# Kernel tuning notes

Measured on AMD Instinct MI355X. Metric: run time of the kernel, lower is better.

Reference implementation:

```python
import jax, jax.numpy as jnp
import numpy as np

B, N, C = 16, 1024, 384
HEADS = 4
HIDDEN = 4 * C  # mlp_ratio=4 -> 1536
EPS = 1e-5


def layernorm(x, g, b):
    mu = jnp.mean(x, axis=-1, keepdims=True)
    var = jnp.mean((x - mu) ** 2, axis=-1, keepdims=True)
    return (x - mu) / jnp.sqrt(var + EPS) * g + b


def hardswish(x):
    return x * jnp.clip(x + 3.0, 0.0, 6.0) / 6.0


def setup_inputs() -> dict:
    key = jax.random.key(0)
    ks = jax.random.split(key, 8)
    s = 0.02
    return {
        "x": jax.random.normal(ks[0], (B, N, C), jnp.float32),
        "ln1_g": jnp.ones((C,), jnp.float32),
        "ln1_b": jnp.zeros((C,), jnp.float32),
        "Wqkv": jax.random.normal(ks[1], (3 * C, C), jnp.float32) * s,
        "Wproj": jax.random.normal(ks[2], (C, C), jnp.float32) * s,
        "bproj": jnp.zeros((C,), jnp.float32),
        "ln2_g": jnp.ones((C,), jnp.float32),
        "ln2_b": jnp.zeros((C,), jnp.float32),
        "Wfc1": jax.random.normal(ks[3], (HIDDEN, C, 1, 1), jnp.float32) * s,
        "bfc1": jnp.zeros((HIDDEN,), jnp.float32),
        "Wdw": jax.random.normal(ks[4], (HIDDEN, 1, 3, 3), jnp.float32) * s,
        "bdw": jnp.zeros((HIDDEN,), jnp.float32),
        "Wfc2": jax.random.normal(ks[5], (C, HIDDEN, 1, 1), jnp.float32) * s,
        "bfc2": jnp.zeros((C,), jnp.float32),
        "H": 32,
        "W": 32,
    }


def reference(x, ln1_g, ln1_b, Wqkv, Wproj, bproj, ln2_g, ln2_b,
              Wfc1, bfc1, Wdw, bdw, Wfc2, bfc2, H, W):
    b, n, c = x.shape
    h = HEADS
    hd = c // h
    # --- attention branch ---
    xn = layernorm(x, ln1_g, ln1_b)
    qkv = xn @ Wqkv.T  # [B,N,3C]
    qkv = qkv.reshape(b, n, h, 3, hd).transpose(3, 0, 2, 1, 4)  # [3,B,h,N,hd]
    q, k, v = qkv[0], qkv[1], qkv[2]
    attn = jax.nn.softmax(jnp.einsum('bhnd,bhmd->bhnm', q, k) * (hd ** -0.5), axis=-1)
    o = jnp.einsum('bhnm,bhmd->bhnd', attn, v)  # [B,h,N,hd]
    o = o.transpose(0, 2, 1, 3).reshape(b, n, c)
    o = o @ Wproj.T + bproj
    x = x + o
    # --- IRB (inverted residual conv MLP) branch ---
    y = layernorm(x, ln2_g, ln2_b)
    y = y.transpose(0, 2, 1).reshape(b, c, H, W)  # NCHW
    dn = ('NCHW', 'OIHW', 'NCHW')
    y = jax.lax.conv_general_dilated(y, Wfc1, (1, 1), 'VALID', dimension_numbers=dn)
    y = hardswish(y + bfc1[None, :, None, None])
    y = jax.lax.conv_general_dilated(y, Wdw, (1, 1), 'SAME',
                                     feature_group_count=Wdw.shape[0],
                                     dimension_numbers=dn)
    y = hardswish(y + bdw[None, :, None, None])
    y = jax.lax.conv_general_dilated(y, Wfc2, (1, 1), 'VALID', dimension_numbers=dn)
    y = y + bfc2[None, :, None, None]
    y = y.reshape(b, c, n).transpose(0, 2, 1)
    return x + y
```

## Files before the change

### kernel.cpp

```cpp
#include <hip/hip_runtime.h>
#include <hip/hip_bf16.h>
#include <math.h>

#define BB 16
#define NN 1024
#define CC 384
#define HEADS 4
#define HD 96
#define HID 1536
#define MROWS (BB*NN)

typedef __attribute__((ext_vector_type(8))) short bf16x8;
typedef __attribute__((ext_vector_type(4))) float f32x4;

__device__ __forceinline__ float hswish(float x) {
    float t = fminf(fmaxf(x + 3.0f, 0.0f), 6.0f);
    return x * t * (1.0f / 6.0f);
}

__device__ __forceinline__ ushort f2bf(float f) {
    union { float f; unsigned u; } v; v.f = f;
    unsigned r = v.u + 0x7fff + ((v.u >> 16) & 1);
    return (ushort)(r >> 16);
}

__device__ __forceinline__ float bf2f(ushort u) {
    union { unsigned u; float f; } v; v.u = ((unsigned)u) << 16;
    return v.f;
}

__device__ __forceinline__ void gload16(const ushort* g, ushort* l) {
    __builtin_amdgcn_global_load_lds(
        (const __attribute__((address_space(1))) void*)g,
        (__attribute__((address_space(3))) void*)l, 16, 0, 0);
}

__global__ __launch_bounds__(256) void wconv(const float* __restrict__ s,
                                             ushort* __restrict__ d, int n) {
    int i = blockIdx.x * 256 + threadIdx.x;
    if (i < n) d[i] = f2bf(s[i]);
}

__global__ __launch_bounds__(256) void wconv_qkv(const float* __restrict__ s,
                                                 ushort* __restrict__ d) {
    int i = blockIdx.x * 256 + threadIdx.x;
    if (i < 1152 * 384) {
        int row = i / 384;
        float v = s[i];
        if ((row % 288) < 96) v *= 0.10206207261596577f;
        d[i] = f2bf(v);
    }
}

__global__ __launch_bounds__(256) void ln_kernel(
    const float* __restrict__ x, const float* __restrict__ g,
    const float* __restrict__ b, ushort* __restrict__ y)
{
    int row = blockIdx.x * 4 + (threadIdx.x >> 6);
    int lane = threadIdx.x & 63;
    const float* xr = x + (size_t)row * CC;
    float v[6];
    float s = 0.f;
#pragma unroll
    for (int j = 0; j < 6; ++j) { v[j] = xr[lane + 64 * j]; s += v[j]; }
#pragma unroll
    for (int off = 32; off; off >>= 1) s += __shfl_xor(s, off, 64);
    float mu = s * (1.0f / CC);
    float s2 = 0.f;
#pragma unroll
    for (int j = 0; j < 6; ++j) { float d = v[j] - mu; s2 += d * d; }
#pragma unroll
    for (int off = 32; off; off >>= 1) s2 += __shfl_xor(s2, off, 64);
    float rinv = rsqrtf(s2 * (1.0f / CC) + 1e-5f);
    ushort* yr = y + (size_t)row * CC;
#pragma unroll
    for (int j = 0; j < 6; ++j) {
        int c = lane + 64 * j;
        yr[c] = f2bf((v[j] - mu) * rinv * g[c] + b[c]);
    }
}

template<int BN>
__global__ __launch_bounds__(256) void gemm_mfma(
    const ushort* __restrict__ A, const ushort* __restrict__ B,
    const float* __restrict__ bias, const float* __restrict__ res,
    float* __restrict__ Cf, ushort* __restrict__ Cb,
    int M, int N, int K, int act)
{
    constexpr int NF = BN / 32;
    __shared__ ushort As[128][64];
    __shared__ ushort Bs[BN][64];
    int tid = threadIdx.x;
    int lane = tid & 63, w = tid >> 6;
    int wr = w >> 1, wc = w & 1;
    int g = lane >> 4, li = lane & 15;

    int nx = N / BN;
    int bid = blockIdx.x;
    int rr = bid & 7, qq = bid >> 3;
    int xx = qq % nx, yy = (qq / nx) * 8 + rr;
    int m0 = yy * 128, n0 = xx * BN;

    int srow = tid >> 3;
    int scol = ((tid & 7) ^ (srow & 7)) * 8;

    f32x4 acc[4][NF];
#pragma unroll
    for (int m = 0; m < 4; ++m)
#pragma unroll
        for (int n = 0; n < NF; ++n) acc[m][n] = (f32x4){0.f, 0.f, 0.f, 0.f};

    for (int k0 = 0; k0 < K; k0 += 64) {
        __syncthreads();
#pragma unroll
        for (int j = 0; j < 4; ++j)
            gload16(A + (size_t)(m0 + j * 32 + srow) * K + k0 + scol,
                    &As[j * 32 + w * 8][0]);
#pragma unroll
        for (int j = 0; j < BN / 32; ++j)
            gload16(B + (size_t)(n0 + j * 32 + srow) * K + k0 + scol,
                    &Bs[j * 32 + w * 8][0]);
        __syncthreads();
#pragma unroll
        for (int s = 0; s < 2; ++s) {
            bf16x8 af[4], bfr[NF];
#pragma unroll
            for (int m = 0; m < 4; ++m) {
                int row = wr * 64 + m * 16 + li;
                af[m] = *(const bf16x8*)&As[row][((s * 4 + g) ^ (row & 7)) * 8];
            }
#pragma unroll
            for (int n = 0; n < NF; ++n) {
                int row = wc * (BN / 2) + n * 16 + li;
                bfr[n] = *(const bf16x8*)&Bs[row][((s * 4 + g) ^ (row & 7)) * 8];
            }
            __builtin_amdgcn_s_setprio(1);
#pragma unroll
            for (int m = 0; m < 4; ++m)
#pragma unroll
                for (int n = 0; n < NF; ++n)
                    acc[m][n] = __builtin_amdgcn_mfma_f32_16x16x32_bf16(
                        af[m], bfr[n], acc[m][n], 0, 0, 0);
            __builtin_amdgcn_s_setprio(0);
        }
    }

#pragma unroll
    for (int m = 0; m < 4; ++m)
#pragma unroll
        for (int n = 0; n < NF; ++n) {
            int col = n0 + wc * (BN / 2) + n * 16 + li;
            float bv = bias ? bias[col] : 0.f;
#pragma unroll
            for (int r = 0; r < 4; ++r) {
                int row = m0 + wr * 64 + m * 16 + g * 4 + r;
                float v = acc[m][n][r] + bv;
                if (act == 1) v = hswish(v);
                if (res) v += res[(size_t)row * N + col];
                if (Cb) Cb[(size_t)row * N + col] = f2bf(v);
                else    Cf[(size_t)row * N + col] = v;
            }
        }
}

__global__ __launch_bounds__(256) void gemm_qkv(
    const ushort* __restrict__ A, const ushort* __restrict__ B,
    ushort* __restrict__ Qb, ushort* __restrict__ Kb, ushort* __restrict__ Vb,
    int M)
{
    constexpr int K = CC;
    __shared__ ushort As[128][64];
    __shared__ ushort Bs[128][64];
    int tid = threadIdx.x;
    int lane = tid & 63, w = tid >> 6;
    int wr = w >> 1, wc = w & 1;
    int g = lane >> 4, li = lane & 15;

    const int nx = 1152 / 128;
    int bid = blockIdx.x;
    int rr = bid & 7, qq = bid >> 3;
    int xx = qq % nx, yy = (qq / nx) * 8 + rr;
    int m0 = yy * 128, n0 = xx * 128;

    int srow = tid >> 3;
    int scol = ((tid & 7) ^ (srow & 7)) * 8;

    f32x4 acc[4][4];
#pragma unroll
    for (int m = 0; m < 4; ++m)
#pragma unroll
        for (int n = 0; n < 4; ++n) acc[m][n] = (f32x4){0.f, 0.f, 0.f, 0.f};

    for (int k0 = 0; k0 < K; k0 += 64) {
        __syncthreads();
#pragma unroll
        for (int j = 0; j < 4; ++j) {
            gload16(A + (size_t)(m0 + j * 32 + srow) * K + k0 + scol,
                    &As[j * 32 + w * 8][0]);
            gload16(B + (size_t)(n0 + j * 32 + srow) * K + k0 + scol,
                    &Bs[j * 32 + w * 8][0]);
        }
        __syncthreads();
#pragma unroll
        for (int s = 0; s < 2; ++s) {
            bf16x8 af[4], bfr[4];
#pragma unroll
            for (int m = 0; m < 4; ++m) {
                int row = wr * 64 + m * 16 + li;
                af[m] = *(const bf16x8*)&As[row][((s * 4 + g) ^ (row & 7)) * 8];
            }
#pragma unroll
            for (int n = 0; n < 4; ++n) {
                int row = wc * 64 + n * 16 + li;
                bfr[n] = *(const bf16x8*)&Bs[row][((s * 4 + g) ^ (row & 7)) * 8];
            }
            __builtin_amdgcn_s_setprio(1);
#pragma unroll
            for (int m = 0; m < 4; ++m)
#pragma unroll
                for (int n = 0; n < 4; ++n)
                    acc[m][n] = __builtin_amdgcn_mfma_f32_16x16x32_bf16(
                        af[m], bfr[n], acc[m][n], 0, 0, 0);
            __builtin_amdgcn_s_setprio(0);
        }
    }

#pragma unroll
    for (int m = 0; m < 4; ++m)
#pragma unroll
        for (int n = 0; n < 4; ++n) {
            int col = n0 + wc * 64 + n * 16 + li;
            int h = col / 288;
            int rem = col - h * 288;
            int which = rem / 96;
            int d = rem - which * 96;
            ushort* dst = which == 0 ? Qb : (which == 1 ? Kb : Vb);
#pragma unroll
            for (int r = 0; r < 4; ++r) {
                int row = m0 + wr * 64 + m * 16 + g * 4 + r;
                int b = row >> 10, ntok = row & 1023;
                int bh = b * HEADS + h;
                dst[((size_t)bh * NN + ntok) * HD + d] = f2bf(acc[m][n][r]);
            }
        }
}

__global__ __launch_bounds__(256) void conv_v(
    const ushort* __restrict__ Vb, ushort* __restrict__ Vt)
{
    __shared__ ushort vt[HD][136];
    int n0 = blockIdx.x * 128;
    int bh = blockIdx.y;
    const ushort* base = Vb + ((size_t)bh * NN + n0) * HD;
    for (int i = threadIdx.x; i < 128 * HD; i += 256) {
        int n = i / HD, d = i % HD;
        vt[d][n] = base[(size_t)n * HD + d];
    }
    __syncthreads();
    for (int i = threadIdx.x; i < HD * 128; i += 256) {
        int d = i / 128, n = i % 128;
        Vt[((size_t)bh * HD + d) * NN + n0 + n] = vt[d][n];
    }
}

#define KVT 64
#define KPAD 104
#define VPAD 72
#define PPAD 72

__global__ __launch_bounds__(256) void attn_mfma(
    const ushort* __restrict__ Qb, const ushort* __restrict__ Kb,
    const ushort* __restrict__ Vt, ushort* __restrict__ o)
{
    __shared__ ushort Klds[KVT][KPAD];
    __shared__ ushort Vlds[112][VPAD];
    __shared__ ushort Plds[4][16][PPAD];
    int tid = threadIdx.x;
    int lane = tid & 63, w = tid >> 6;
    int g = lane >> 4, li = lane & 15;
    int bid = blockIdx.x;
    int qt = bid >> 6, bh = bid & 63;
    int q0 = qt * 64;
    int b = bh >> 2, h = bh & 3;

    for (int i = tid; i < 16 * VPAD; i += 256) {
        int rr = i / VPAD, cc = i % VPAD;
        Vlds[96 + rr][cc] = (rr == 0 && cc < 64) ? (ushort)0x3F80 : (ushort)0;
    }

    const ushort* qrow = Qb + ((size_t)bh * NN + q0 + w * 16 + li) * HD;
    bf16x8 qf[3];
#pragma unroll
    for (int s = 0; s < 3; ++s)
        qf[s] = *(const bf16x8*)(qrow + s * 32 + g * 8);

    f32x4 oacc[7];
#pragma unroll
    for (int dt = 0; dt < 7; ++dt) oacc[dt] = (f32x4){0.f, 0.f, 0.f, 0.f};

    for (int t = 0; t < NN / KVT; ++t) {
        int n0 = t * KVT;
        __syncthreads();
        for (int i = tid; i < KVT * 12; i += 256) {
            int row = i / 12, ch = i % 12;
            *(bf16x8*)&Klds[row][ch * 8] =
                *(const bf16x8*)(Kb + ((size_t)bh * NN + n0 + row) * HD + ch * 8);
        }
        for (int i = tid; i < HD * 8; i += 256) {
            int d = i / 8, ch = i % 8;
            *(bf16x8*)&Vlds[d][ch * 8] =
                *(const bf16x8*)(Vt + ((size_t)bh * HD + d) * NN + n0 + ch * 8);
        }
        __syncthreads();

        f32x4 sacc[4];
#pragma unroll
        for (int c = 0; c < 4; ++c) sacc[c] = (f32x4){0.f, 0.f, 0.f, 0.f};
        __builtin_amdgcn_s_setprio(1);
#pragma unroll
        for (int s = 0; s < 3; ++s)
#pragma unroll
            for (int c = 0; c < 4; ++c) {
                bf16x8 kf = *(const bf16x8*)&Klds[c * 16 + li][s * 32 + g * 8];
                sacc[c] = __builtin_amdgcn_mfma_f32_16x16x32_bf16(qf[s], kf, sacc[c], 0, 0, 0);
            }
        __builtin_amdgcn_s_setprio(0);

#pragma unroll
        for (int r = 0; r < 4; ++r)
#pragma unroll
            for (int c = 0; c < 4; ++c)
                Plds[w][g * 4 + r][c * 16 + li] = f2bf(__expf(sacc[c][r]));

        __builtin_amdgcn_s_setprio(1);
#pragma unroll
        for (int sub = 0; sub < 2; ++sub) {
            bf16x8 pf = *(const bf16x8*)&Plds[w][li][sub * 32 + g * 8];
#pragma unroll
            for (int dt = 0; dt < 7; ++dt) {
                bf16x8 vf = *(const bf16x8*)&Vlds[dt * 16 + li][sub * 32 + g * 8];
                oacc[dt] = __builtin_amdgcn_mfma_f32_16x16x32_bf16(pf, vf, oacc[dt], 0, 0, 0);
            }
        }
        __builtin_amdgcn_s_setprio(0);
    }

    float inv[4];
#pragma unroll
    for (int r = 0; r < 4; ++r)
        inv[r] = 1.0f / __shfl(oacc[6][r], lane & 48, 64);
#pragma unroll
    for (int dt = 0; dt < 6; ++dt)
#pragma unroll
        for (int r = 0; r < 4; ++r) {
            int row = q0 + w * 16 + g * 4 + r;
            int col = h * HD + dt * 16 + li;
            o[(size_t)(b * NN + row) * CC + col] = f2bf(oacc[dt][r] * inv[r]);
        }
}

__global__ __launch_bounds__(256) void dw_kernel(
    const ushort* __restrict__ h1, const float* __restrict__ w,
    const float* __restrict__ bias, ushort* __restrict__ h2)
{
    int tid = threadIdx.x;
    int c0 = blockIdx.x * 128 + (tid & 63) * 2;
    int x = blockIdx.y * 4 + (tid >> 6);
    int b = blockIdx.z;
    const ushort* base = h1 + (size_t)b * NN * HID + c0;
    ushort* obase = h2 + (size_t)b * NN * HID + c0;

    float wA[9], wB[9];
#pragma unroll
    for (int k = 0; k < 9; ++k) {
        wA[k] = w[c0 * 9 + k];
        wB[k] = w[(c0 + 1) * 9 + k];
    }
    float bA = bias[c0], bB = bias[c0 + 1];

    bool xm = (x > 0), xp = (x < 31);

    float m0a = 0, m0b = 0, m1a = 0, m1b = 0, m2a = 0, m2b = 0;
    float c0a = 0, c0b = 0, c1a = 0, c1b = 0, c2a = 0, c2b = 0;

    {
        if (xm) { ushort2 u = *(const ushort2*)&base[(size_t)(x - 1) * HID]; c0a = bf2f(u.x); c0b = bf2f(u.y); }
        { ushort2 u = *(const ushort2*)&base[(size_t)x * HID]; c1a = bf2f(u.x); c1b = bf2f(u.y); }
        if (xp) { ushort2 u = *(const ushort2*)&base[(size_t)(x + 1) * HID]; c2a = bf2f(u.x); c2b = bf2f(u.y); }
    }

#pragma unroll
    for (int y = 0; y < 32; ++y) {
        float n0a = 0, n0b = 0, n1a = 0, n1b = 0, n2a = 0, n2b = 0;
        if (y < 31) {
            const ushort* rp = base + (size_t)((y + 1) * 32 + x) * HID;
            if (xm) { ushort2 u = *(const ushort2*)(rp - HID); n0a = bf2f(u.x); n0b = bf2f(u.y); }
            { ushort2 u = *(const ushort2*)rp; n1a = bf2f(u.x); n1b = bf2f(u.y); }
            if (xp) { ushort2 u = *(const ushort2*)(rp + HID); n2a = bf2f(u.x); n2b = bf2f(u.y); }
        }
        float aA = bA, aB = bB;
        aA = fmaf(m0a, wA[0], aA); aB = fmaf(m0b, wB[0], aB);
        aA = fmaf(m1a, wA[1], aA); aB = fmaf(m1b, wB[1], aB);
        aA = fmaf(m2a, wA[2], aA); aB = fmaf(m2b, wB[2], aB);
        aA = fmaf(c0a, wA[3], aA); aB = fmaf(c0b, wB[3], aB);
        aA = fmaf(c1a, wA[4], aA); aB = fmaf(c1b, wB[4], aB);
        aA = fmaf(c2a, wA[5], aA); aB = fmaf(c2b, wB[5], aB);
        aA = fmaf(n0a, wA[6], aA); aB = fmaf(n0b, wB[6], aB);
        aA = fmaf(n1a, wA[7], aA); aB = fmaf(n1b, wB[7], aB);
        aA = fmaf(n2a, wA[8], aA); aB = fmaf(n2b, wB[8], aB);
        ushort2 ov;
        ov.x = f2bf(hswish(aA));
        ov.y = f2bf(hswish(aB));
        *(ushort2*)&obase[(size_t)(y * 32 + x) * HID] = ov;
        m0a = c0a; m0b = c0b; m1a = c1a; m1b = c1b; m2a = c2a; m2b = c2b;
        c0a = n0a; c0b = n0b; c1a = n1a; c1b = n1b; c2a = n2a; c2b = n2b;
    }
}

extern "C" void kernel_launch(void* const* d_in, const int* in_sizes, int n_in,
                              void* d_out, int out_size, void* d_ws, size_t ws_size,
                              hipStream_t stream) {
    const float* x     = (const float*)d_in[0];
    const float* ln1_g = (const float*)d_in[1];
    const float* ln1_b = (const float*)d_in[2];
    const float* Wqkv  = (const float*)d_in[3];
    const float* Wproj = (const float*)d_in[4];
    const float* bproj = (const float*)d_in[5];
    const float* ln2_g = (const float*)d_in[6];
    const float* ln2_b = (const float*)d_in[7];
    const float* Wfc1  = (const float*)d_in[8];
    const float* bfc1  = (const float*)d_in[9];
    const float* Wdw   = (const float*)d_in[10];
    const float* bdw   = (const float*)d_in[11];
    const float* Wfc2  = (const float*)d_in[12];
    const float* bfc2  = (const float*)d_in[13];
    float* out = (float*)d_out;

    const int M = MROWS;
    ushort* abuf = (ushort*)d_ws;
    ushort* Qb   = abuf + (size_t)M * 384;
    ushort* Kb   = Qb   + (size_t)M * 384;
    ushort* Vb   = Kb   + (size_t)M * 384;
    ushort* Vt   = Vb   + (size_t)M * 384;
    ushort* obuf = Vt   + (size_t)M * 384;
    ushort* h1   = obuf + (size_t)M * 384;
    ushort* h2   = h1   + (size_t)M * 1536;
    ushort* wq   = h2   + (size_t)M * 1536;
    ushort* wp   = wq   + 1152 * 384;
    ushort* w1   = wp   + 384 * 384;
    ushort* w2   = w1   + 1536 * 384;

    wconv_qkv<<<(1152 * 384 + 255) / 256, 256, 0, stream>>>(Wqkv, wq);
    wconv<<<(384 * 384 + 255) / 256, 256, 0, stream>>>(Wproj, wp, 384 * 384);
    wconv<<<(1536 * 384 + 255) / 256, 256, 0, stream>>>(Wfc1, w1, 1536 * 384);
    wconv<<<(384 * 1536 + 255) / 256, 256, 0, stream>>>(Wfc2, w2, 384 * 1536);

    ln_kernel<<<M / 4, 256, 0, stream>>>(x, ln1_g, ln1_b, abuf);
    gemm_qkv<<<(1152 / 128) * (M / 128), 256, 0, stream>>>(abuf, wq, Qb, Kb, Vb, M);
    conv_v<<<dim3(NN / 128, BB * HEADS), 256, 0, stream>>>(Vb, Vt);
    attn_mfma<<<1024, 256, 0, stream>>>(Qb, Kb, Vt, obuf);
    gemm_mfma<64><<<(CC / 64) * (M / 128), 256, 0, stream>>>(
        obuf, wp, bproj, x, out, nullptr, M, CC, CC, 0);
    ln_kernel<<<M / 4, 256, 0, stream>>>(out, ln2_g, ln2_b, abuf);
    gemm_mfma<128><<<(HID / 128) * (M / 128), 256, 0, stream>>>(
        abuf, w1, bfc1, nullptr, nullptr, h1, M, HID, CC, 1);
    dw_kernel<<<dim3(HID / 128, 8, BB), 256, 0, stream>>>(h1, Wdw, bdw, h2);
    gemm_mfma<64><<<(CC / 64) * (M / 128), 256, 0, stream>>>(
        h2, w2, bfc2, out, out, nullptr, M, CC, HID, 0);
}
```

Measured before the change: 250.1 us.

## Fuse V transpose into QKV GEMM, stage bf16 epilogues via LDS, merge weight casts

The QKV GEMM now tiles N by 96 so each block covers exactly one head's Q, K or V slice. It stages results in LDS and writes Q/K rows with vector stores, and V already transposed. This removes the separate conv_v kernel and the Vb intermediate buffer. The bf16-output GEMM epilogue also goes through a swizzled LDS tile for coalesced 16-byte stores, the four weight-conversion kernels become one launch, and the attention softmax uses exp2f with the Q scale folded in log2e. The extra LDS round trips and barriers add some epilogue cost, and the exp2 rescale must exactly match the old scaling.

Measured after the change: 263.2 us. 1.05x slower.

```diff
diff --git a/kernel.cpp b/kernel.cpp
--- a/kernel.cpp
+++ b/kernel.cpp
@@ -35,21 +35,30 @@
         (__attribute__((address_space(3))) void*)l, 16, 0, 0);
 }
 
-__global__ __launch_bounds__(256) void wconv(const float* __restrict__ s,
-                                             ushort* __restrict__ d, int n) {
+#define S_QKV (1152*384)
+#define S_P   (384*384)
+#define S_1   (1536*384)
+#define S_2   (384*1536)
+__global__ __launch_bounds__(256) void wconv_all(
+    const float* __restrict__ wqkv, const float* __restrict__ wproj,
+    const float* __restrict__ wfc1, const float* __restrict__ wfc2,
+    ushort* __restrict__ dq, ushort* __restrict__ dp,
+    ushort* __restrict__ d1, ushort* __restrict__ d2)
+{
     int i = blockIdx.x * 256 + threadIdx.x;
-    if (i < n) d[i] = f2bf(s[i]);
-}
-
-__global__ __launch_bounds__(256) void wconv_qkv(const float* __restrict__ s,
-                                                 ushort* __restrict__ d) {
-    int i = blockIdx.x * 256 + threadIdx.x;
-    if (i < 1152 * 384) {
+    if (i < S_QKV) {
         int row = i / 384;
-        float v = s[i];
-        if ((row % 288) < 96) v *= 0.10206207261596577f;
-        d[i] = f2bf(v);
-    }
+        float v = wqkv[i];
+        if ((row % 288) < 96) v *= 0.14724615088646412f;
+        dq[i] = f2bf(v);
+        return;
+    }
+    i -= S_QKV;
+    if (i < S_P) { dp[i] = f2bf(wproj[i]); return; }
+    i -= S_P;
+    if (i < S_1) { d1[i] = f2bf(wfc1[i]); return; }
+    i -= S_1;
+    if (i < S_2) d2[i] = f2bf(wfc2[i]);
 }
 
 __global__ __launch_bounds__(256) void ln_kernel(
@@ -88,8 +97,10 @@
     int M, int N, int K, int act)
 {
     constexpr int NF = BN / 32;
-    __shared__ ushort As[128][64];
-    __shared__ ushort Bs[BN][64];
+    __shared__ ushort sh[128 * 64 + BN * 64];
+    ushort* As = sh;
+    ushort* Bs = sh + 128 * 64;
+    ushort* Ct = sh;
     int tid = threadIdx.x;
     int lane = tid & 63, w = tid >> 6;
     int wr = w >> 1, wc = w & 1;
@@ -115,11 +126,11 @@
 #pragma unroll
         for (int j = 0; j < 4; ++j)
             gload16(A + (size_t)(m0 + j * 32 + srow) * K + k0 + scol,
-                    &As[j * 32 + w * 8][0]);
+                    &As[(j * 32 + w * 8) * 64]);
 #pragma unroll
         for (int j = 0; j < BN / 32; ++j)
             gload16(B + (size_t)(n0 + j * 32 + srow) * K + k0 + scol,
-                    &Bs[j * 32 + w * 8][0]);
+                    &Bs[(j * 32 + w * 8) * 64]);
         __syncthreads();
 #pragma unroll
         for (int s = 0; s < 2; ++s) {
@@ -127,12 +138,12 @@
 #pragma unroll
             for (int m = 0; m < 4; ++m) {
                 int row = wr * 64 + m * 16 + li;
-                af[m] = *(const bf16x8*)&As[row][((s * 4 + g) ^ (row & 7)) * 8];
+                af[m] = *(const bf16x8*)&As[row * 64 + ((s * 4 + g) ^ (row & 7)) * 8];
             }
 #pragma unroll
             for (int n = 0; n < NF; ++n) {
                 int row = wc * (BN / 2) + n * 16 + li;
-                bfr[n] = *(const bf16x8*)&Bs[row][((s * 4 + g) ^ (row & 7)) * 8];
+                bfr[n] = *(const bf16x8*)&Bs[row * 64 + ((s * 4 + g) ^ (row & 7)) * 8];
             }
             __builtin_amdgcn_s_setprio(1);
 #pragma unroll
@@ -145,121 +156,160 @@
         }
     }
 
-#pragma unroll
-    for (int m = 0; m < 4; ++m)
-#pragma unroll
-        for (int n = 0; n < NF; ++n) {
-            int col = n0 + wc * (BN / 2) + n * 16 + li;
-            float bv = bias ? bias[col] : 0.f;
-#pragma unroll
-            for (int r = 0; r < 4; ++r) {
-                int row = m0 + wr * 64 + m * 16 + g * 4 + r;
-                float v = acc[m][n][r] + bv;
-                if (act == 1) v = hswish(v);
-                if (res) v += res[(size_t)row * N + col];
-                if (Cb) Cb[(size_t)row * N + col] = f2bf(v);
-                else    Cf[(size_t)row * N + col] = v;
-            }
-        }
+    if (Cb) {
+        __syncthreads();
+#pragma unroll
+        for (int m = 0; m < 4; ++m)
+#pragma unroll
+            for (int n = 0; n < NF; ++n) {
+                int lc = wc * (BN / 2) + n * 16 + li;
+                int col = n0 + lc;
+                float bv = bias ? bias[col] : 0.f;
+#pragma unroll
+                for (int r = 0; r < 4; ++r) {
+                    int row = wr * 64 + m * 16 + g * 4 + r;
+                    float v = acc[m][n][r] + bv;
+                    if (act == 1) v = hswish(v);
+                    if (res) v += res[(size_t)(m0 + row) * N + col];
+                    Ct[row * BN + ((lc >> 3) ^ (row & 7)) * 8 + (li & 7)] = f2bf(v);
+                }
+            }
+        __syncthreads();
+        int u = tid >> 1, e = tid & 1;
+#pragma unroll
+        for (int j = 0; j < BN / 16; ++j) {
+            int chunk = e * (BN / 16) + j;
+            bf16x8 val = *(const bf16x8*)&Ct[u * BN + (chunk ^ (u & 7)) * 8];
+            *(bf16x8*)(Cb + (size_t)(m0 + u) * N + n0 + chunk * 8) = val;
+        }
+    } else {
+#pragma unroll
+        for (int m = 0; m < 4; ++m)
+#pragma unroll
+            for (int n = 0; n < NF; ++n) {
+                int col = n0 + wc * (BN / 2) + n * 16 + li;
+                float bv = bias ? bias[col] : 0.f;
+#pragma unroll
+                for (int r = 0; r < 4; ++r) {
+                    int row = m0 + wr * 64 + m * 16 + g * 4 + r;
+                    float v = acc[m][n][r] + bv;
+                    if (act == 1) v = hswish(v);
+                    if (res) v += res[(size_t)row * N + col];
+                    Cf[(size_t)row * N + col] = v;
+                }
+            }
+    }
 }
 
 __global__ __launch_bounds__(256) void gemm_qkv(
     const ushort* __restrict__ A, const ushort* __restrict__ B,
-    ushort* __restrict__ Qb, ushort* __restrict__ Kb, ushort* __restrict__ Vb,
+    ushort* __restrict__ Qb, ushort* __restrict__ Kb, ushort* __restrict__ Vt,
     int M)
 {
     constexpr int K = CC;
-    __shared__ ushort As[128][64];
-    __shared__ ushort Bs[128][64];
+    __shared__ ushort sh[128 * 64 + 96 * 64];
+    ushort* As = sh;
+    ushort* Bs = sh + 128 * 64;
+    ushort* Ct = sh;
     int tid = threadIdx.x;
     int lane = tid & 63, w = tid >> 6;
     int wr = w >> 1, wc = w & 1;
     int g = lane >> 4, li = lane & 15;
 
-    const int nx = 1152 / 128;
+    const int nx = 12;
     int bid = blockIdx.x;
     int rr = bid & 7, qq = bid >> 3;
     int xx = qq % nx, yy = (qq / nx) * 8 + rr;
-    int m0 = yy * 128, n0 = xx * 128;
+    int m0 = yy * 128, n0 = xx * 96;
+    int h = xx / 3, which = xx % 3;
 
     int srow = tid >> 3;
     int scol = ((tid & 7) ^ (srow & 7)) * 8;
 
-    f32x4 acc[4][4];
+    f32x4 acc[4][3];
 #pragma unroll
     for (int m = 0; m < 4; ++m)
 #pragma unroll
-        for (int n = 0; n < 4; ++n) acc[m][n] = (f32x4){0.f, 0.f, 0.f, 0.f};
+        for (int n = 0; n < 3; ++n) acc[m][n] = (f32x4){0.f, 0.f, 0.f, 0.f};
 
     for (int k0 = 0; k0 < K; k0 += 64) {
         __syncthreads();
 #pragma unroll
-        for (int j = 0; j < 4; ++j) {
+        for (int j = 0; j < 4; ++j)
             gload16(A + (size_t)(m0 + j * 32 + srow) * K + k0 + scol,
-                    &As[j * 32 + w * 8][0]);
+                    &As[(j * 32 + w * 8) * 64]);
+#pragma unroll
+        for (int j = 0; j < 3; ++j)
             gload16(B + (size_t)(n0 + j * 32 + srow) * K + k0 + scol,
-                    &Bs[j * 32 + w * 8][0]);
-        }
+                    &Bs[(j * 32 + w * 8) * 64]);
         __syncthreads();
 #pragma unroll
         for (int s = 0; s < 2; ++s) {
-            bf16x8 af[4], bfr[4];
+            bf16x8 af[4], bfr[3];
 #pragma unroll
             for (int m = 0; m < 4; ++m) {
                 int row = wr * 64 + m * 16 + li;
-                af[m] = *(const bf16x8*)&As[row][((s * 4 + g) ^ (row & 7)) * 8];
-            }
-#pragma unroll
-            for (int n = 0; n < 4; ++n) {
-                int row = wc * 64 + n * 16 + li;
-                bfr[n] = *(const bf16x8*)&Bs[row][((s * 4 + g) ^ (row & 7)) * 8];
+                af[m] = *(const bf16x8*)&As[row * 64 + ((s * 4 + g) ^ (row & 7)) * 8];
+            }
+#pragma unroll
+            for (int n = 0; n < 3; ++n) {
+                int row = wc * 48 + n * 16 + li;
+                bfr[n] = *(const bf16x8*)&Bs[row * 64 + ((s * 4 + g) ^ (row & 7)) * 8];
             }
             __builtin_amdgcn_s_setprio(1);
 #pragma unroll
             for (int m = 0; m < 4; ++m)
 #pragma unroll
-                for (int n = 0; n < 4; ++n)
+                for (int n = 0; n < 3; ++n)
                     acc[m][n] = __builtin_amdgcn_mfma_f32_16x16x32_bf16(
                         af[m], bfr[n], acc[m][n], 0, 0, 0);
             __builtin_amdgcn_s_setprio(0);
         }
     }
 
+    __syncthreads();
 #pragma unroll
     for (int m = 0; m < 4; ++m)
 #pragma unroll
-        for (int n = 0; n < 4; ++n) {
-            int col = n0 + wc * 64 + n * 16 + li;
-            int h = col / 288;
-            int rem = col - h * 288;
-            int which = rem / 96;
-            int d = rem - which * 96;
-            ushort* dst = which == 0 ? Qb : (which == 1 ? Kb : Vb);
+        for (int n = 0; n < 3; ++n) {
+            int lc = wc * 48 + n * 16 + li;
+            int chunk = lc >> 3;
 #pragma unroll
             for (int r = 0; r < 4; ++r) {
-                int row = m0 + wr * 64 + m * 16 + g * 4 + r;
-                int b = row >> 10, ntok = row & 1023;
-                int bh = b * HEADS + h;
-                dst[((size_t)bh * NN + ntok) * HD + d] = f2bf(acc[m][n][r]);
-            }
-        }
-}
-
-__global__ __launch_bounds__(256) void conv_v(
-    const ushort* __restrict__ Vb, ushort* __restrict__ Vt)
-{
-    __shared__ ushort vt[HD][136];
-    int n0 = blockIdx.x * 128;
-    int bh = blockIdx.y;
-    const ushort* base = Vb + ((size_t)bh * NN + n0) * HD;
-    for (int i = threadIdx.x; i < 128 * HD; i += 256) {
-        int n = i / HD, d = i % HD;
-        vt[d][n] = base[(size_t)n * HD + d];
-    }
+                int row = wr * 64 + m * 16 + g * 4 + r;
+                Ct[row * 96 + (chunk ^ (row & 3)) * 8 + (li & 7)] = f2bf(acc[m][n][r]);
+            }
+        }
     __syncthreads();
-    for (int i = threadIdx.x; i < HD * 128; i += 256) {
-        int d = i / 128, n = i % 128;
-        Vt[((size_t)bh * HD + d) * NN + n0 + n] = vt[d][n];
+
+    if (which < 2) {
+        ushort* dst = which == 0 ? Qb : Kb;
+        int u = tid >> 1, e = tid & 1;
+        int tok = m0 + u;
+        int b = tok >> 10, ntok = tok & 1023;
+        int bh = b * HEADS + h;
+        ushort* drow = dst + ((size_t)bh * NN + ntok) * HD;
+#pragma unroll
+        for (int j = 0; j < 6; ++j) {
+            int chunk = e * 6 + j;
+            bf16x8 val = *(const bf16x8*)&Ct[u * 96 + (chunk ^ (u & 3)) * 8];
+            *(bf16x8*)(drow + chunk * 8) = val;
+        }
+    } else {
+        int b = m0 >> 10, ntok0 = m0 & 1023;
+        int bh = b * HEADS + h;
+#pragma unroll
+        for (int it = 0; it < 6; ++it) {
+            int idx = it * 256 + tid;
+            int d = idx >> 4, u0 = (idx & 15) * 8;
+            ushort tmp[8];
+#pragma unroll
+            for (int e2 = 0; e2 < 8; ++e2) {
+                int row = u0 + e2;
+                tmp[e2] = Ct[row * 96 + ((d >> 3) ^ (row & 3)) * 8 + (d & 7)];
+            }
+            *(bf16x8*)(Vt + ((size_t)bh * HD + d) * NN + ntok0 + u0) = *(bf16x8*)tmp;
+        }
     }
 }
 
@@ -330,7 +380,7 @@
         for (int r = 0; r < 4; ++r)
 #pragma unroll
             for (int c = 0; c < 4; ++c)
-                Plds[w][g * 4 + r][c * 16 + li] = f2bf(__expf(sacc[c][r]));
+                Plds[w][g * 4 + r][c * 16 + li] = f2bf(exp2f(sacc[c][r]));
 
         __builtin_amdgcn_s_setprio(1);
 #pragma unroll
@@ -440,8 +490,7 @@
     ushort* abuf = (ushort*)d_ws;
     ushort* Qb   = abuf + (size_t)M * 384;
     ushort* Kb   = Qb   + (size_t)M * 384;
-    ushort* Vb   = Kb   + (size_t)M * 384;
-    ushort* Vt   = Vb   + (size_t)M * 384;
+    ushort* Vt   = Kb   + (size_t)M * 384;
     ushort* obuf = Vt   + (size_t)M * 384;
     ushort* h1   = obuf + (size_t)M * 384;
     ushort* h2   = h1   + (size_t)M * 1536;
@@ -450,14 +499,11 @@
     ushort* w1   = wp   + 384 * 384;
     ushort* w2   = w1   + 1536 * 384;
 
-    wconv_qkv<<<(1152 * 384 + 255) / 256, 256, 0, stream>>>(Wqkv, wq);
-    wconv<<<(384 * 384 + 255) / 256, 256, 0, stream>>>(Wproj, wp, 384 * 384);
-    wconv<<<(1536 * 384 + 255) / 256, 256, 0, stream>>>(Wfc1, w1, 1536 * 384);
-    wconv<<<(384 * 1536 + 255) / 256, 256, 0, stream>>>(Wfc2, w2, 384 * 1536);
+    wconv_all<<<(S_QKV + S_P + S_1 + S_2 + 255) / 256, 256, 0, stream>>>(
+        Wqkv, Wproj, Wfc1, Wfc2, wq, wp, w1, w2);
 
     ln_kernel<<<M / 4, 256, 0, stream>>>(x, ln1_g, ln1_b, abuf);
-    gemm_qkv<<<(1152 / 128) * (M / 128), 256, 0, stream>>>(abuf, wq, Qb, Kb, Vb, M);
-    conv_v<<<dim3(NN / 128, BB * HEADS), 256, 0, stream>>>(Vb, Vt);
+    gemm_qkv<<<12 * (M / 128), 256, 0, stream>>>(abuf, wq, Qb, Kb, Vt, M);
     attn_mfma<<<1024, 256, 0, stream>>>(Qb, Kb, Vt, obuf);
     gemm_mfma<64><<<(CC / 64) * (M / 128), 256, 0, stream>>>(
         obuf, wp, bproj, x, out, nullptr, M, CC, CC, 0);
```
